# Kernel optimization log

Measured on AMD Instinct MI355X. Metric: run time of the kernel, lower is better.

## Reference

```python
import jax, jax.numpy as jnp
import numpy as np

C = 768
R = 16
H = C // R  # 48


def setup_inputs() -> dict:
    key = jax.random.key(0)
    ks = jax.random.split(key, 5)
    x = jax.random.normal(ks[0], (32, 64, 64, C), dtype=jnp.float32)
    # Xavier-uniform linear weights (stored as [in, out] for jnp.dot)
    lim1 = float(np.sqrt(6.0 / (C + H)))
    W1 = jax.random.uniform(ks[1], (C, H), dtype=jnp.float32, minval=-lim1, maxval=lim1)
    b1 = jax.random.normal(ks[2], (H,), dtype=jnp.float32) * 1e-6
    lim2 = float(np.sqrt(6.0 / (H + C)))
    W2 = jax.random.uniform(ks[3], (H, C), dtype=jnp.float32, minval=-lim2, maxval=lim2)
    b2 = jax.random.normal(ks[4], (C,), dtype=jnp.float32) * 1e-6
    gamma = jnp.ones((C,), dtype=jnp.float32)
    beta = jnp.zeros((C,), dtype=jnp.float32)
    return {"x": x, "W1": W1, "b1": b1, "W2": W2, "b2": b2, "gamma": gamma, "beta": beta}


def _layernorm(x, gamma, beta, eps=1e-5):
    mu = jnp.mean(x, axis=-1, keepdims=True)
    var = jnp.mean(jnp.square(x - mu), axis=-1, keepdims=True)
    return (x - mu) * jax.lax.rsqrt(var + eps) * gamma + beta


def reference(x, W1, b1, W2, b2, gamma, beta):
    # x: [b, h, w, c]; LayerNorm over c, bottleneck MLP, residual add.
    out1 = _layernorm(x, gamma, beta)
    hid = out1 @ W1 + b1                       # [b,h,w,H]
    hid = hid * jax.nn.sigmoid(1.702 * hid)    # QuickGELU
    out = hid @ W2 + b2                        # [b,h,w,c]
    return x + out
```

## Files before the change

kernel.cpp:

```cpp
#include <hip/hip_runtime.h>
#include <hip/hip_bf16.h>
#include <stdint.h>

#define CDIM 768
#define HDIM 48

typedef float  f32x4  __attribute__((ext_vector_type(4)));
typedef short  bf16x8 __attribute__((ext_vector_type(8)));
typedef unsigned short u16x4 __attribute__((ext_vector_type(4)));

__device__ __forceinline__ unsigned short f2bf(float x) {
    __hip_bfloat16 h = __float2bfloat16(x);
    return *reinterpret_cast<unsigned short*>(&h);
}

__global__ __launch_bounds__(256) void prep_kernel(
    const float* __restrict__ W1, const float* __restrict__ b1,
    const float* __restrict__ W2,
    const float* __restrict__ gamma, const float* __restrict__ beta,
    unsigned short* __restrict__ w1p, unsigned short* __restrict__ w2p,
    float* __restrict__ b1p, float* __restrict__ cs1)
{
    const int blk = blockIdx.x, tid = threadIdx.x;
    const int l = tid & 63;
    if (blk < 18) {
        const int fid = blk * 4 + (tid >> 6);
        const int kt = fid / 3, nt = fid % 3;
        const int k0 = kt * 32 + 8 * (l >> 4);
        const int n  = nt * 16 + (l & 15);
        bf16x8 v;
        #pragma unroll
        for (int b = 0; b < 8; ++b) {
            const int k = k0 + b;
            v[b] = (short)f2bf(gamma[k] * W1[k * HDIM + n]);
        }
        *reinterpret_cast<bf16x8*>(w1p + (size_t)(fid * 64 + l) * 8) = v;
    } else if (blk < 42) {
        const int fid = (blk - 18) * 4 + (tid >> 6);
        const int kt = fid / 48, nt = fid % 48;
        const int k0 = kt * 32 + 8 * (l >> 4);
        const int n  = nt * 16 + (l & 15);
        bf16x8 v;
        #pragma unroll
        for (int b = 0; b < 8; ++b) {
            const int k = k0 + b;
            const float w = (k < HDIM) ? W2[k * CDIM + n] : 0.0f;
            v[b] = (short)f2bf(w);
        }
        *reinterpret_cast<bf16x8*>(w2p + (size_t)(fid * 64 + l) * 8) = v;
    } else {
        const int j = tid >> 2, p = tid & 3;
        float sb = 0.f, sg = 0.f;
        if (j < HDIM) {
            for (int c = p * 192; c < (p + 1) * 192; ++c) {
                const float w = W1[c * HDIM + j];
                sb += beta[c]  * w;
                sg += gamma[c] * w;
            }
        }
        sb += __shfl_xor(sb, 1); sb += __shfl_xor(sb, 2);
        sg += __shfl_xor(sg, 1); sg += __shfl_xor(sg, 2);
        if (p == 0 && j < HDIM) { b1p[j] = b1[j] + sb; cs1[j] = sg; }
    }
}

__global__ __launch_bounds__(256, 2) void mlp_kernel(
    const float* __restrict__ x,
    const float* __restrict__ b2g,
    const unsigned short* __restrict__ w1p,
    const unsigned short* __restrict__ w2p,
    const float* __restrict__ b1p,
    const float* __restrict__ cs1,
    float* __restrict__ out)
{
    __shared__ __align__(16) char  lds_big[73728];
    __shared__ __align__(16) float lds_b2[CDIM];
    __shared__ __align__(16) float lds_b1[HDIM];
    __shared__ __align__(16) float lds_cs[HDIM];

    const int tid  = threadIdx.x;
    const int w    = tid >> 6;
    const int l    = tid & 63;
    const int lrow = l & 15;
    const int lg   = l >> 4;

    if (tid < 192)       reinterpret_cast<f32x4*>(lds_b2)[tid]       = reinterpret_cast<const f32x4*>(b2g)[tid];
    else if (tid < 204)  reinterpret_cast<f32x4*>(lds_b1)[tid - 192] = reinterpret_cast<const f32x4*>(b1p)[tid - 192];
    else if (tid < 216)  reinterpret_cast<f32x4*>(lds_cs)[tid - 204] = reinterpret_cast<const f32x4*>(cs1)[tid - 204];

    {
        const f32x4* __restrict__ src = reinterpret_cast<const f32x4*>(w1p);
        f32x4* __restrict__ dst = reinterpret_cast<f32x4*>(lds_big);
        #pragma unroll
        for (int i = 0; i < 18; ++i)
            dst[tid + i * 256] = src[tid + i * 256];
    }
    __syncthreads();

    const bf16x8* __restrict__ w1l = reinterpret_cast<const bf16x8*>(lds_big);
    const bf16x8* __restrict__ w2f = reinterpret_cast<const bf16x8*>(w2p);

    const int    tile = blockIdx.x * 4 + w;
    const size_t m0   = (size_t)tile * 16;
    const float* __restrict__ xrow = x + (m0 + lrow) * CDIM + 8 * lg;

    f32x4 acc1[3];
    #pragma unroll
    for (int nt = 0; nt < 3; ++nt) { acc1[nt][0]=0.f; acc1[nt][1]=0.f; acc1[nt][2]=0.f; acc1[nt][3]=0.f; }
    float rs0 = 0.f, rs1 = 0.f, rq0 = 0.f, rq1 = 0.f;

    #pragma unroll 1
    for (int ch = 0; ch < 6; ++ch) {
        f32x4 xv[8];
        #pragma unroll
        for (int j = 0; j < 8; ++j)
            xv[j] = *reinterpret_cast<const f32x4*>(xrow + ch * 128 + (j >> 1) * 32 + (j & 1) * 4);

        #pragma unroll
        for (int ktl = 0; ktl < 4; ++ktl) {
            const int kt = ch * 4 + ktl;
            const bf16x8 wv0 = w1l[(kt * 3 + 0) * 64 + l];
            const bf16x8 wv1 = w1l[(kt * 3 + 1) * 64 + l];
            const bf16x8 wv2 = w1l[(kt * 3 + 2) * 64 + l];
            const f32x4 xa = xv[2 * ktl + 0];
            const f32x4 xb = xv[2 * ktl + 1];
            bf16x8 bf;
            #pragma unroll
            for (int b = 0; b < 4; ++b) {
                if (b & 1) { rs1 += xa[b]; rq1 += xa[b] * xa[b]; rs1 += xb[b]; rq1 += xb[b] * xb[b]; }
                else       { rs0 += xa[b]; rq0 += xa[b] * xa[b]; rs0 += xb[b]; rq0 += xb[b] * xb[b]; }
                bf[b]     = (short)f2bf(xa[b]);
                bf[b + 4] = (short)f2bf(xb[b]);
            }
            acc1[0] = __builtin_amdgcn_mfma_f32_16x16x32_bf16(wv0, bf, acc1[0], 0, 0, 0);
            acc1[1] = __builtin_amdgcn_mfma_f32_16x16x32_bf16(wv1, bf, acc1[1], 0, 0, 0);
            acc1[2] = __builtin_amdgcn_mfma_f32_16x16x32_bf16(wv2, bf, acc1[2], 0, 0, 0);
        }
    }

    float rsum = rs0 + rs1, rsq = rq0 + rq1;
    rsum += __shfl_xor(rsum, 16); rsum += __shfl_xor(rsum, 32);
    rsq  += __shfl_xor(rsq , 16); rsq  += __shfl_xor(rsq , 32);
    const float mu   = rsum * (1.f / 768.f);
    const float var  = rsq * (1.f / 768.f) - mu * mu;
    const float rstd = rsqrtf(var + 1e-5f);

    __syncthreads();

    unsigned short* const hid = reinterpret_cast<unsigned short*>(lds_big);
    *reinterpret_cast<unsigned long long*>(hid + ((w * 16 + (l >> 2)) * 72) + 48 + (l & 3) * 4) = 0ull;

    #pragma unroll
    for (int nt = 0; nt < 3; ++nt) {
        const int c4 = nt * 16 + 4 * lg;
        const f32x4 bb = *reinterpret_cast<const f32x4*>(&lds_b1[c4]);
        const f32x4 cs = *reinterpret_cast<const f32x4*>(&lds_cs[c4]);
        u16x4 pk;
        #pragma unroll
        for (int r = 0; r < 4; ++r) {
            const float h = rstd * (acc1[nt][r] - mu * cs[r]) + bb[r];
            const float g = h / (1.f + __expf(-1.702f * h));
            pk[r] = f2bf(g);
        }
        *reinterpret_cast<u16x4*>(hid + (w * 16 + lrow) * 72 + c4) = pk;
    }
    const bf16x8 a2_0 = *reinterpret_cast<const bf16x8*>(hid + (w * 16 + lrow) * 72 + 8 * lg);
    const bf16x8 a2_1 = *reinterpret_cast<const bf16x8*>(hid + (w * 16 + lrow) * 72 + 8 * lg + 32);

    const float* __restrict__ xres = x   + (m0 + lrow) * CDIM;
    float* __restrict__       ores = out + (m0 + lrow) * CDIM;

    #pragma unroll 1
    for (int ch = 0; ch < 6; ++ch) {
        f32x4 res[8];
        #pragma unroll
        for (int n8 = 0; n8 < 8; ++n8)
            res[n8] = *reinterpret_cast<const f32x4*>(xres + (ch * 8 + n8) * 16 + 4 * lg);
        f32x4 acc2[8];
        #pragma unroll
        for (int n8 = 0; n8 < 8; ++n8) { acc2[n8][0]=0.f; acc2[n8][1]=0.f; acc2[n8][2]=0.f; acc2[n8][3]=0.f; }
        #pragma unroll
        for (int n8 = 0; n8 < 8; ++n8) {
            const int ct = ch * 8 + n8;
            acc2[n8] = __builtin_amdgcn_mfma_f32_16x16x32_bf16(w2f[ct * 64 + l],        a2_0, acc2[n8], 0, 0, 0);
            acc2[n8] = __builtin_amdgcn_mfma_f32_16x16x32_bf16(w2f[(48 + ct) * 64 + l], a2_1, acc2[n8], 0, 0, 0);
        }
        #pragma unroll
        for (int n8 = 0; n8 < 8; ++n8) {
            const int c4 = (ch * 8 + n8) * 16 + 4 * lg;
            const f32x4 bb = *reinterpret_cast<const f32x4*>(&lds_b2[c4]);
            f32x4 o;
            #pragma unroll
            for (int r = 0; r < 4; ++r) o[r] = acc2[n8][r] + bb[r] + res[n8][r];
            *reinterpret_cast<f32x4*>(ores + c4) = o;
        }
    }
}

extern "C" void kernel_launch(void* const* d_in, const int* in_sizes, int n_in,
                              void* d_out, int out_size, void* d_ws, size_t ws_size,
                              hipStream_t stream)
{
    const float* x     = (const float*)d_in[0];
    const float* W1    = (const float*)d_in[1];
    const float* b1    = (const float*)d_in[2];
    const float* W2    = (const float*)d_in[3];
    const float* b2    = (const float*)d_in[4];
    const float* gamma = (const float*)d_in[5];
    const float* beta  = (const float*)d_in[6];
    float* out = (float*)d_out;

    unsigned short* w1p = (unsigned short*)d_ws;
    unsigned short* w2p = w1p + 24 * 3 * 64 * 8;
    float* b1p = (float*)(w2p + 2 * 48 * 64 * 8);
    float* cs1 = b1p + 64;

    const int M = in_sizes[0] / CDIM;
    const int blocks = M / 64;

    prep_kernel<<<dim3(43), dim3(256), 0, stream>>>(W1, b1, W2, gamma, beta, w1p, w2p, b1p, cs1);
    mlp_kernel<<<dim3(blocks), dim3(256), 0, stream>>>(x, b2, w1p, w2p, b1p, cs1, out);
}
```

Before: 254.2 us.

## Persistent waves software-pipeline GEMM2 of one tile with GEMM1 of next

Blocks grow to 512 threads (8 waves) and each wave now processes four 16-row tiles in a strided persistent loop. The GEMM2/residual store of the current tile is interleaved with the x loads and GEMM1 of the next tile, so memory and MFMA work overlap within a wave. The W1 LDS copy is amortized over 8x fewer blocks, and a separate hidden-activation LDS buffer removes the block-wide barrier before the epilogue. The cost is higher register pressure from holding two tiles' state, and fewer blocks (M/512) that may underfill CUs or leave a tail imbalance.

```diff
diff --git a/kernel.cpp b/kernel.cpp
--- a/kernel.cpp
+++ b/kernel.cpp
@@ -64,7 +64,42 @@
     }
 }
 
-__global__ __launch_bounds__(256, 2) void mlp_kernel(
+__device__ __forceinline__ void g1_finalize(
+    const f32x4& a0, const f32x4& a1, const f32x4& a2in,
+    float rsum, float rsq,
+    const float* __restrict__ lds_b1, const float* __restrict__ lds_cs,
+    unsigned short* __restrict__ hidslot,
+    int lrow, int lg, int l,
+    bf16x8& a2_0, bf16x8& a2_1)
+{
+    rsum += __shfl_xor(rsum, 16); rsum += __shfl_xor(rsum, 32);
+    rsq  += __shfl_xor(rsq , 16); rsq  += __shfl_xor(rsq , 32);
+    const float mu   = rsum * (1.f / 768.f);
+    const float var  = rsq * (1.f / 768.f) - mu * mu;
+    const float rstd = rsqrtf(var + 1e-5f);
+
+    *reinterpret_cast<unsigned long long*>(hidslot + (l >> 2) * 72 + 48 + (l & 3) * 4) = 0ull;
+
+    const f32x4 accs[3] = {a0, a1, a2in};
+    #pragma unroll
+    for (int nt = 0; nt < 3; ++nt) {
+        const int c4 = nt * 16 + 4 * lg;
+        const f32x4 bb = *reinterpret_cast<const f32x4*>(&lds_b1[c4]);
+        const f32x4 cs = *reinterpret_cast<const f32x4*>(&lds_cs[c4]);
+        u16x4 pk;
+        #pragma unroll
+        for (int r = 0; r < 4; ++r) {
+            const float h = rstd * (accs[nt][r] - mu * cs[r]) + bb[r];
+            const float g = h / (1.f + __expf(-1.702f * h));
+            pk[r] = f2bf(g);
+        }
+        *reinterpret_cast<u16x4*>(hidslot + lrow * 72 + c4) = pk;
+    }
+    a2_0 = *reinterpret_cast<const bf16x8*>(hidslot + lrow * 72 + 8 * lg);
+    a2_1 = *reinterpret_cast<const bf16x8*>(hidslot + lrow * 72 + 8 * lg + 32);
+}
+
+__global__ __launch_bounds__(512, 2) void mlp_kernel(
     const float* __restrict__ x,
     const float* __restrict__ b2g,
     const unsigned short* __restrict__ w1p,
@@ -73,7 +108,8 @@
     const float* __restrict__ cs1,
     float* __restrict__ out)
 {
-    __shared__ __align__(16) char  lds_big[73728];
+    __shared__ __align__(16) char  lds_w1[73728];
+    __shared__ __align__(16) unsigned short lds_hid[8][16][72];
     __shared__ __align__(16) float lds_b2[CDIM];
     __shared__ __align__(16) float lds_b1[HDIM];
     __shared__ __align__(16) float lds_cs[HDIM];
@@ -87,112 +123,164 @@
     if (tid < 192)       reinterpret_cast<f32x4*>(lds_b2)[tid]       = reinterpret_cast<const f32x4*>(b2g)[tid];
     else if (tid < 204)  reinterpret_cast<f32x4*>(lds_b1)[tid - 192] = reinterpret_cast<const f32x4*>(b1p)[tid - 192];
     else if (tid < 216)  reinterpret_cast<f32x4*>(lds_cs)[tid - 204] = reinterpret_cast<const f32x4*>(cs1)[tid - 204];
-
     {
         const f32x4* __restrict__ src = reinterpret_cast<const f32x4*>(w1p);
-        f32x4* __restrict__ dst = reinterpret_cast<f32x4*>(lds_big);
-        #pragma unroll
-        for (int i = 0; i < 18; ++i)
-            dst[tid + i * 256] = src[tid + i * 256];
+        f32x4* __restrict__ dst = reinterpret_cast<f32x4*>(lds_w1);
+        #pragma unroll
+        for (int i = 0; i < 9; ++i)
+            dst[tid + i * 512] = src[tid + i * 512];
     }
     __syncthreads();
 
-    const bf16x8* __restrict__ w1l = reinterpret_cast<const bf16x8*>(lds_big);
+    const bf16x8* __restrict__ w1l = reinterpret_cast<const bf16x8*>(lds_w1);
     const bf16x8* __restrict__ w2f = reinterpret_cast<const bf16x8*>(w2p);
-
-    const int    tile = blockIdx.x * 4 + w;
-    const size_t m0   = (size_t)tile * 16;
-    const float* __restrict__ xrow = x + (m0 + lrow) * CDIM + 8 * lg;
-
-    f32x4 acc1[3];
-    #pragma unroll
-    for (int nt = 0; nt < 3; ++nt) { acc1[nt][0]=0.f; acc1[nt][1]=0.f; acc1[nt][2]=0.f; acc1[nt][3]=0.f; }
-    float rs0 = 0.f, rs1 = 0.f, rq0 = 0.f, rq1 = 0.f;
+    unsigned short* const hidslot = &lds_hid[w][0][0];
+
+    const int waveId  = blockIdx.x * 8 + w;
+    const int wstride = gridDim.x * 8;
+
+    size_t m0c = (size_t)waveId * 16;
+    bf16x8 a2_0c, a2_1c;
+
+    {
+        const float* __restrict__ xrow = x + (m0c + lrow) * CDIM + 8 * lg;
+        f32x4 acc1[3];
+        #pragma unroll
+        for (int nt = 0; nt < 3; ++nt) { acc1[nt][0]=0.f; acc1[nt][1]=0.f; acc1[nt][2]=0.f; acc1[nt][3]=0.f; }
+        float rsum = 0.f, rsq = 0.f;
+        #pragma unroll 1
+        for (int ch = 0; ch < 6; ++ch) {
+            f32x4 xv[8];
+            #pragma unroll
+            for (int j = 0; j < 8; ++j)
+                xv[j] = *reinterpret_cast<const f32x4*>(xrow + ch * 128 + (j >> 1) * 32 + (j & 1) * 4);
+            #pragma unroll
+            for (int ktl = 0; ktl < 4; ++ktl) {
+                const int kt = ch * 4 + ktl;
+                const bf16x8 wv0 = w1l[(kt * 3 + 0) * 64 + l];
+                const bf16x8 wv1 = w1l[(kt * 3 + 1) * 64 + l];
+                const bf16x8 wv2 = w1l[(kt * 3 + 2) * 64 + l];
+                const f32x4 xa = xv[2 * ktl + 0];
+                const f32x4 xb = xv[2 * ktl + 1];
+                bf16x8 bf;
+                #pragma unroll
+                for (int b = 0; b < 4; ++b) {
+                    rsum += xa[b]; rsq += xa[b] * xa[b];
+                    rsum += xb[b]; rsq += xb[b] * xb[b];
+                    bf[b]     = (short)f2bf(xa[b]);
+                    bf[b + 4] = (short)f2bf(xb[b]);
+                }
+                acc1[0] = __builtin_amdgcn_mfma_f32_16x16x32_bf16(wv0, bf, acc1[0], 0, 0, 0);
+                acc1[1] = __builtin_amdgcn_mfma_f32_16x16x32_bf16(wv1, bf, acc1[1], 0, 0, 0);
+                acc1[2] = __builtin_amdgcn_mfma_f32_16x16x32_bf16(wv2, bf, acc1[2], 0, 0, 0);
+            }
+        }
+        g1_finalize(acc1[0], acc1[1], acc1[2], rsum, rsq, lds_b1, lds_cs,
+                    hidslot, lrow, lg, l, a2_0c, a2_1c);
+    }
 
     #pragma unroll 1
-    for (int ch = 0; ch < 6; ++ch) {
-        f32x4 xv[8];
-        #pragma unroll
-        for (int j = 0; j < 8; ++j)
-            xv[j] = *reinterpret_cast<const f32x4*>(xrow + ch * 128 + (j >> 1) * 32 + (j & 1) * 4);
-
-        #pragma unroll
-        for (int ktl = 0; ktl < 4; ++ktl) {
-            const int kt = ch * 4 + ktl;
-            const bf16x8 wv0 = w1l[(kt * 3 + 0) * 64 + l];
-            const bf16x8 wv1 = w1l[(kt * 3 + 1) * 64 + l];
-            const bf16x8 wv2 = w1l[(kt * 3 + 2) * 64 + l];
-            const f32x4 xa = xv[2 * ktl + 0];
-            const f32x4 xb = xv[2 * ktl + 1];
-            bf16x8 bf;
-            #pragma unroll
-            for (int b = 0; b < 4; ++b) {
-                if (b & 1) { rs1 += xa[b]; rq1 += xa[b] * xa[b]; rs1 += xb[b]; rq1 += xb[b] * xb[b]; }
-                else       { rs0 += xa[b]; rq0 += xa[b] * xa[b]; rs0 += xb[b]; rq0 += xb[b] * xb[b]; }
-                bf[b]     = (short)f2bf(xa[b]);
-                bf[b + 4] = (short)f2bf(xb[b]);
-            }
-            acc1[0] = __builtin_amdgcn_mfma_f32_16x16x32_bf16(wv0, bf, acc1[0], 0, 0, 0);
-            acc1[1] = __builtin_amdgcn_mfma_f32_16x16x32_bf16(wv1, bf, acc1[1], 0, 0, 0);
-            acc1[2] = __builtin_amdgcn_mfma_f32_16x16x32_bf16(wv2, bf, acc1[2], 0, 0, 0);
-        }
-    }
-
-    float rsum = rs0 + rs1, rsq = rq0 + rq1;
-    rsum += __shfl_xor(rsum, 16); rsum += __shfl_xor(rsum, 32);
-    rsq  += __shfl_xor(rsq , 16); rsq  += __shfl_xor(rsq , 32);
-    const float mu   = rsum * (1.f / 768.f);
-    const float var  = rsq * (1.f / 768.f) - mu * mu;
-    const float rstd = rsqrtf(var + 1e-5f);
-
-    __syncthreads();
-
-    unsigned short* const hid = reinterpret_cast<unsigned short*>(lds_big);
-    *reinterpret_cast<unsigned long long*>(hid + ((w * 16 + (l >> 2)) * 72) + 48 + (l & 3) * 4) = 0ull;
-
-    #pragma unroll
-    for (int nt = 0; nt < 3; ++nt) {
-        const int c4 = nt * 16 + 4 * lg;
-        const f32x4 bb = *reinterpret_cast<const f32x4*>(&lds_b1[c4]);
-        const f32x4 cs = *reinterpret_cast<const f32x4*>(&lds_cs[c4]);
-        u16x4 pk;
-        #pragma unroll
-        for (int r = 0; r < 4; ++r) {
-            const float h = rstd * (acc1[nt][r] - mu * cs[r]) + bb[r];
-            const float g = h / (1.f + __expf(-1.702f * h));
-            pk[r] = f2bf(g);
-        }
-        *reinterpret_cast<u16x4*>(hid + (w * 16 + lrow) * 72 + c4) = pk;
-    }
-    const bf16x8 a2_0 = *reinterpret_cast<const bf16x8*>(hid + (w * 16 + lrow) * 72 + 8 * lg);
-    const bf16x8 a2_1 = *reinterpret_cast<const bf16x8*>(hid + (w * 16 + lrow) * 72 + 8 * lg + 32);
-
-    const float* __restrict__ xres = x   + (m0 + lrow) * CDIM;
-    float* __restrict__       ores = out + (m0 + lrow) * CDIM;
-
-    #pragma unroll 1
-    for (int ch = 0; ch < 6; ++ch) {
-        f32x4 res[8];
-        #pragma unroll
-        for (int n8 = 0; n8 < 8; ++n8)
-            res[n8] = *reinterpret_cast<const f32x4*>(xres + (ch * 8 + n8) * 16 + 4 * lg);
-        f32x4 acc2[8];
-        #pragma unroll
-        for (int n8 = 0; n8 < 8; ++n8) { acc2[n8][0]=0.f; acc2[n8][1]=0.f; acc2[n8][2]=0.f; acc2[n8][3]=0.f; }
-        #pragma unroll
-        for (int n8 = 0; n8 < 8; ++n8) {
-            const int ct = ch * 8 + n8;
-            acc2[n8] = __builtin_amdgcn_mfma_f32_16x16x32_bf16(w2f[ct * 64 + l],        a2_0, acc2[n8], 0, 0, 0);
-            acc2[n8] = __builtin_amdgcn_mfma_f32_16x16x32_bf16(w2f[(48 + ct) * 64 + l], a2_1, acc2[n8], 0, 0, 0);
-        }
-        #pragma unroll
-        for (int n8 = 0; n8 < 8; ++n8) {
-            const int c4 = (ch * 8 + n8) * 16 + 4 * lg;
-            const f32x4 bb = *reinterpret_cast<const f32x4*>(&lds_b2[c4]);
-            f32x4 o;
-            #pragma unroll
-            for (int r = 0; r < 4; ++r) o[r] = acc2[n8][r] + bb[r] + res[n8][r];
-            *reinterpret_cast<f32x4*>(ores + c4) = o;
+    for (int g = 0; g < 3; ++g) {
+        const size_t m0n = m0c + (size_t)wstride * 16;
+        const float* __restrict__ xres  = x   + (m0c + lrow) * CDIM;
+        float* __restrict__       ores  = out + (m0c + lrow) * CDIM;
+        const float* __restrict__ xrown = x   + (m0n + lrow) * CDIM + 8 * lg;
+
+        f32x4 acc1[3];
+        #pragma unroll
+        for (int nt = 0; nt < 3; ++nt) { acc1[nt][0]=0.f; acc1[nt][1]=0.f; acc1[nt][2]=0.f; acc1[nt][3]=0.f; }
+        float rsum = 0.f, rsq = 0.f;
+
+        #pragma unroll 1
+        for (int cc = 0; cc < 12; ++cc) {
+            bf16x8 w2v[8];
+            #pragma unroll
+            for (int i = 0; i < 4; ++i) {
+                const int ct = cc * 4 + i;
+                w2v[2 * i]     = w2f[ct * 64 + l];
+                w2v[2 * i + 1] = w2f[(48 + ct) * 64 + l];
+            }
+            f32x4 res[4];
+            #pragma unroll
+            for (int i = 0; i < 4; ++i)
+                res[i] = *reinterpret_cast<const f32x4*>(xres + (cc * 4 + i) * 16 + 4 * lg);
+            f32x4 xv[4];
+            #pragma unroll
+            for (int j = 0; j < 4; ++j)
+                xv[j] = *reinterpret_cast<const f32x4*>(xrown + cc * 64 + (j >> 1) * 32 + (j & 1) * 4);
+
+            f32x4 acc2[4];
+            #pragma unroll
+            for (int i = 0; i < 4; ++i) { acc2[i][0]=0.f; acc2[i][1]=0.f; acc2[i][2]=0.f; acc2[i][3]=0.f; }
+            #pragma unroll
+            for (int i = 0; i < 4; ++i) {
+                acc2[i] = __builtin_amdgcn_mfma_f32_16x16x32_bf16(w2v[2 * i],     a2_0c, acc2[i], 0, 0, 0);
+                acc2[i] = __builtin_amdgcn_mfma_f32_16x16x32_bf16(w2v[2 * i + 1], a2_1c, acc2[i], 0, 0, 0);
+            }
+            #pragma unroll
+            for (int i = 0; i < 4; ++i) {
+                const int c4 = (cc * 4 + i) * 16 + 4 * lg;
+                const f32x4 bb = *reinterpret_cast<const f32x4*>(&lds_b2[c4]);
+                f32x4 o;
+                #pragma unroll
+                for (int r = 0; r < 4; ++r) o[r] = acc2[i][r] + bb[r] + res[i][r];
+                *reinterpret_cast<f32x4*>(ores + c4) = o;
+            }
+
+            #pragma unroll
+            for (int ktl = 0; ktl < 2; ++ktl) {
+                const int kt = cc * 2 + ktl;
+                const bf16x8 wv0 = w1l[(kt * 3 + 0) * 64 + l];
+                const bf16x8 wv1 = w1l[(kt * 3 + 1) * 64 + l];
+                const bf16x8 wv2 = w1l[(kt * 3 + 2) * 64 + l];
+                const f32x4 xa = xv[2 * ktl + 0];
+                const f32x4 xb = xv[2 * ktl + 1];
+                bf16x8 bf;
+                #pragma unroll
+                for (int b = 0; b < 4; ++b) {
+                    rsum += xa[b]; rsq += xa[b] * xa[b];
+                    rsum += xb[b]; rsq += xb[b] * xb[b];
+                    bf[b]     = (short)f2bf(xa[b]);
+                    bf[b + 4] = (short)f2bf(xb[b]);
+                }
+                acc1[0] = __builtin_amdgcn_mfma_f32_16x16x32_bf16(wv0, bf, acc1[0], 0, 0, 0);
+                acc1[1] = __builtin_amdgcn_mfma_f32_16x16x32_bf16(wv1, bf, acc1[1], 0, 0, 0);
+                acc1[2] = __builtin_amdgcn_mfma_f32_16x16x32_bf16(wv2, bf, acc1[2], 0, 0, 0);
+            }
+        }
+
+        g1_finalize(acc1[0], acc1[1], acc1[2], rsum, rsq, lds_b1, lds_cs,
+                    hidslot, lrow, lg, l, a2_0c, a2_1c);
+        m0c = m0n;
+    }
+
+    {
+        const float* __restrict__ xres = x   + (m0c + lrow) * CDIM;
+        float* __restrict__       ores = out + (m0c + lrow) * CDIM;
+        #pragma unroll 1
+        for (int ch = 0; ch < 6; ++ch) {
+            f32x4 res[8];
+            #pragma unroll
+            for (int n8 = 0; n8 < 8; ++n8)
+                res[n8] = *reinterpret_cast<const f32x4*>(xres + (ch * 8 + n8) * 16 + 4 * lg);
+            f32x4 acc2[8];
+            #pragma unroll
+            for (int n8 = 0; n8 < 8; ++n8) { acc2[n8][0]=0.f; acc2[n8][1]=0.f; acc2[n8][2]=0.f; acc2[n8][3]=0.f; }
+            #pragma unroll
+            for (int n8 = 0; n8 < 8; ++n8) {
+                const int ct = ch * 8 + n8;
+                acc2[n8] = __builtin_amdgcn_mfma_f32_16x16x32_bf16(w2f[ct * 64 + l],        a2_0c, acc2[n8], 0, 0, 0);
+                acc2[n8] = __builtin_amdgcn_mfma_f32_16x16x32_bf16(w2f[(48 + ct) * 64 + l], a2_1c, acc2[n8], 0, 0, 0);
+            }
+            #pragma unroll
+            for (int n8 = 0; n8 < 8; ++n8) {
+                const int c4 = (ch * 8 + n8) * 16 + 4 * lg;
+                const f32x4 bb = *reinterpret_cast<const f32x4*>(&lds_b2[c4]);
+                f32x4 o;
+                #pragma unroll
+                for (int r = 0; r < 4; ++r) o[r] = acc2[n8][r] + bb[r] + res[n8][r];
+                *reinterpret_cast<f32x4*>(ores + c4) = o;
+            }
         }
     }
 }
@@ -216,8 +304,8 @@
     float* cs1 = b1p + 64;
 
     const int M = in_sizes[0] / CDIM;
-    const int blocks = M / 64;
+    const int blocks = M / 512;
 
     prep_kernel<<<dim3(43), dim3(256), 0, stream>>>(W1, b1, W2, gamma, beta, w1p, w2p, b1p, cs1);
-    mlp_kernel<<<dim3(blocks), dim3(256), 0, stream>>>(x, b2, w1p, w2p, b1p, cs1, out);
-}
+    mlp_kernel<<<dim3(blocks), dim3(512), 0, stream>>>(x, b2, w1p, w2p, b1p, cs1, out);
+}
```

Result: slower. 270.7 us (+6.5%).
